# Performance work log

Measured on AMD Instinct MI355X. Metric: run time of the kernel, lower is better.

The kernel has to match this reference:

```python
import jax, jax.numpy as jnp
import numpy as np

N_NODES = 20000
N_EDGES = 320000


def cheb_conv(x, row, col, W, b):
    """PyG ChebConv with normalization='sym', lambda_max=2.0 (default).
    Scaled Laplacian L~ = L - I = -D^{-1/2} A D^{-1/2} (diagonal cancels:
    get_laplacian diag +1 plus add_self_loops fill -1).
    Tx_0 = x, Tx_1 = L~ x, Tx_k = 2 L~ Tx_{k-1} - Tx_{k-2};
    out = sum_k Tx_k @ W_k + b.
    """
    N = x.shape[0]
    mask = (row != col).astype(x.dtype)  # remove_self_loops
    deg = jax.ops.segment_sum(mask, row, num_segments=N)
    dis = jnp.where(deg > 0, 1.0 / jnp.sqrt(deg), 0.0)  # deg_inv_sqrt, inf->0
    w = -dis[row] * dis[col] * mask  # edge weights of L~ (diag entries are 0)

    def prop(t):  # y = L~ t via gather-scale-scatter over edges
        return jax.ops.segment_sum(w[:, None] * t[col], row, num_segments=N)

    K = W.shape[0]
    Tx0 = x
    out = Tx0 @ W[0]
    Tx1 = prop(Tx0)
    if K > 1:
        out = out + Tx1 @ W[1]
    for k in range(2, K):
        Tx2 = 2.0 * prop(Tx1) - Tx0
        out = out + Tx2 @ W[k]
        Tx0, Tx1 = Tx1, Tx2
    return out + b


def setup_inputs() -> dict:
    key = jax.random.key(0)
    ks = jax.random.split(key, 10)
    x = jax.random.normal(ks[0], (N_NODES, 1152), dtype=jnp.float32)
    row = jax.random.randint(ks[1], (N_EDGES,), 0, N_NODES)
    col = jax.random.randint(ks[2], (N_EDGES,), 0, N_NODES)
    s1 = 1.0 / np.sqrt(1152)
    s2 = 1.0 / np.sqrt(1152)
    s3 = 1.0 / np.sqrt(576)
    W1 = jax.random.normal(ks[3], (6, 1152, 1152), dtype=jnp.float32) * s1
    b1 = jax.random.normal(ks[4], (1152,), dtype=jnp.float32) * 0.01
    W2 = jax.random.normal(ks[5], (5, 1152, 576), dtype=jnp.float32) * s2
    b2 = jax.random.normal(ks[6], (576,), dtype=jnp.float32) * 0.01
    W3 = jax.random.normal(ks[7], (5, 576, 288), dtype=jnp.float32) * s3
    b3 = jax.random.normal(ks[8], (288,), dtype=jnp.float32) * 0.01
    return {"x": x, "row": row, "col": col, "W1": W1, "b1": b1,
            "W2": W2, "b2": b2, "W3": W3, "b3": b3}


def reference(x, row, col, W1, b1, W2, b2, W3, b3):
    # dropout(0.1) is identity in eval mode
    h = jax.nn.relu(cheb_conv(x, row, col, W1, b1))
    h = jax.nn.relu(cheb_conv(h, row, col, W2, b2))
    h = jax.nn.relu(cheb_conv(h, row, col, W3, b3))
    return h
```

## Files before the change

kernel.cpp:

```cpp
#include <hip/hip_runtime.h>
#include <hip/hip_bf16.h>

#define N_NODES 20000
#define N_EDGES 320000

typedef __attribute__((ext_vector_type(8))) short shortx8;
typedef __attribute__((ext_vector_type(4))) float floatx4;
using bf16 = __hip_bfloat16;

typedef __attribute__((address_space(1))) const unsigned int GuT;
typedef __attribute__((address_space(3))) unsigned int LuT;
__device__ __forceinline__ void gl2lds16(const bf16* g, bf16* l) {
  __builtin_amdgcn_global_load_lds((GuT*)g, (LuT*)l, 16, 0, 0);
}

__device__ inline float b2f(unsigned short u) {
  union { unsigned int i; float f; } x;
  x.i = ((unsigned int)u) << 16;
  return x.f;
}
__device__ inline unsigned short f2b(float f) {
  bf16 h(f);
  return *(unsigned short*)&h;
}

struct APtrs { const bf16* p[6]; };


__global__ void zero_kernel(int* p, int n) {
  int i = blockIdx.x * 256 + threadIdx.x;
  if (i < n) p[i] = 0;
}

__global__ void deg_kernel(const int* __restrict__ row, const int* __restrict__ col,
                           int* __restrict__ deg, int nE) {
  int e = blockIdx.x * 256 + threadIdx.x;
  if (e >= nE) return;
  int r = row[e], c = col[e];
  if (r != c) atomicAdd(&deg[r], 1);
}

__global__ void dis_kernel(const int* __restrict__ deg, float* __restrict__ dis, int n) {
  int i = blockIdx.x * 256 + threadIdx.x;
  if (i >= n) return;
  int d = deg[i];
  dis[i] = (d > 0) ? (1.0f / sqrtf((float)d)) : 0.0f;
}

__global__ __launch_bounds__(1024) void scan_kernel(const int* __restrict__ deg,
                                                    int* __restrict__ row_ptr,
                                                    int* __restrict__ cursor, int n) {
  __shared__ int part[1024];
  int t = threadIdx.x;
  int base = t * 20;
  int loc[20];
  int s = 0;
#pragma unroll
  for (int i = 0; i < 20; i++) {
    int idx = base + i;
    int v = (idx < n) ? deg[idx] : 0;
    loc[i] = s;
    s += v;
  }
  part[t] = s;
  __syncthreads();
  for (int offd = 1; offd < 1024; offd <<= 1) {
    int v = (t >= offd) ? part[t - offd] : 0;
    __syncthreads();
    part[t] += v;
    __syncthreads();
  }
  int basev = (t > 0) ? part[t - 1] : 0;
#pragma unroll
  for (int i = 0; i < 20; i++) {
    int idx = base + i;
    if (idx < n) {
      int rp = basev + loc[i];
      row_ptr[idx] = rp;
      cursor[idx] = rp;
    }
  }
  if (t == 1023) row_ptr[n] = part[1023];
}

__global__ void scatter_kernel(const int* __restrict__ row, const int* __restrict__ col,
                               const float* __restrict__ dis, int* __restrict__ cursor,
                               int* __restrict__ col_s, float* __restrict__ w_s, int nE) {
  int e = blockIdx.x * 256 + threadIdx.x;
  if (e >= nE) return;
  int r = row[e], c = col[e];
  if (r == c) return;
  int p = atomicAdd(&cursor[r], 1);
  col_s[p] = c;
  w_s[p] = -dis[r] * dis[c];
}


__global__ void wtrans_kernel(const float* __restrict__ W, bf16* __restrict__ Wt,
                              int K_, int I, int J) {
  __shared__ float tile[32][33];
  int jt = blockIdx.x % (J / 32);
  int rest = blockIdx.x / (J / 32);
  int it = rest % (I / 32);
  int k = rest / (I / 32);
  int tx = threadIdx.x, ty = threadIdx.y;
  const float* src = W + (size_t)k * I * J;
  for (int r = ty; r < 32; r += 8)
    tile[r][tx] = src[(size_t)(it * 32 + r) * J + jt * 32 + tx];
  __syncthreads();
  for (int r = ty; r < 32; r += 8) {
    int j = jt * 32 + r;
    Wt[((size_t)k * J + j) * I + it * 32 + tx] = bf16(tile[tx][r]);
  }
}


__global__ void cast_x_kernel(const float* __restrict__ x, bf16* __restrict__ dst, int n4) {
  int idx = blockIdx.x * 256 + threadIdx.x;
  if (idx >= n4) return;
  int flat = idx * 4;
  float4 v = *(const float4*)(x + flat);
  dst[flat + 0] = bf16(v.x);
  dst[flat + 1] = bf16(v.y);
  dst[flat + 2] = bf16(v.z);
  dst[flat + 3] = bf16(v.w);
}


template <int F, int VEC>
__global__ __launch_bounds__(320) void prop_kernel(
    const int* __restrict__ row_ptr, const int* __restrict__ col_s,
    const float* __restrict__ w_s, const bf16* __restrict__ src,
    const bf16* tx0, bf16* dst) {
  constexpr int C = F / VEC;
  int node = blockIdx.x;
  int t = threadIdx.x;
  bool act = t < C;
  int fb = t * VEC;
  int e0 = row_ptr[node], e1 = row_ptr[node + 1];
  float acc[VEC];
#pragma unroll
  for (int q = 0; q < VEC; q++) acc[q] = 0.0f;

  const unsigned short* sp = (const unsigned short*)src;
  int e = e0;
  for (; e + 16 <= e1; e += 16) {
    int cs[16];
    float wv[16];
#pragma unroll
    for (int u = 0; u < 16; u++) {
      cs[u] = col_s[e + u];
      wv[u] = w_s[e + u];
    }
    if (act) {
      if constexpr (VEC == 4) {
        ushort4 v[16];
#pragma unroll
        for (int u = 0; u < 16; u++) v[u] = *(const ushort4*)(sp + (size_t)cs[u] * F + fb);
#pragma unroll
        for (int u = 0; u < 16; u++) {
          acc[0] += wv[u] * b2f(v[u].x);
          acc[1] += wv[u] * b2f(v[u].y);
          acc[2] += wv[u] * b2f(v[u].z);
          acc[3] += wv[u] * b2f(v[u].w);
        }
      } else {
        ushort2 v[16];
#pragma unroll
        for (int u = 0; u < 16; u++) v[u] = *(const ushort2*)(sp + (size_t)cs[u] * F + fb);
#pragma unroll
        for (int u = 0; u < 16; u++) {
          acc[0] += wv[u] * b2f(v[u].x);
          acc[1] += wv[u] * b2f(v[u].y);
        }
      }
    }
  }
  for (; e + 4 <= e1; e += 4) {
    int cs[4];
    float wv[4];
#pragma unroll
    for (int u = 0; u < 4; u++) {
      cs[u] = col_s[e + u];
      wv[u] = w_s[e + u];
    }
    if (act) {
      if constexpr (VEC == 4) {
        ushort4 v[4];
#pragma unroll
        for (int u = 0; u < 4; u++) v[u] = *(const ushort4*)(sp + (size_t)cs[u] * F + fb);
#pragma unroll
        for (int u = 0; u < 4; u++) {
          acc[0] += wv[u] * b2f(v[u].x);
          acc[1] += wv[u] * b2f(v[u].y);
          acc[2] += wv[u] * b2f(v[u].z);
          acc[3] += wv[u] * b2f(v[u].w);
        }
      } else {
        ushort2 v[4];
#pragma unroll
        for (int u = 0; u < 4; u++) v[u] = *(const ushort2*)(sp + (size_t)cs[u] * F + fb);
#pragma unroll
        for (int u = 0; u < 4; u++) {
          acc[0] += wv[u] * b2f(v[u].x);
          acc[1] += wv[u] * b2f(v[u].y);
        }
      }
    }
  }
  for (; e < e1; e++) {
    int c = col_s[e];
    float w = w_s[e];
    if (act) {
      if constexpr (VEC == 4) {
        ushort4 v = *(const ushort4*)(sp + (size_t)c * F + fb);
        acc[0] += w * b2f(v.x);
        acc[1] += w * b2f(v.y);
        acc[2] += w * b2f(v.z);
        acc[3] += w * b2f(v.w);
      } else {
        ushort2 v = *(const ushort2*)(sp + (size_t)c * F + fb);
        acc[0] += w * b2f(v.x);
        acc[1] += w * b2f(v.y);
      }
    }
  }

  if (!act) return;
  unsigned short* dp = (unsigned short*)dst + (size_t)node * F + fb;
  if (tx0) {
    const unsigned short* t0 = (const unsigned short*)tx0 + (size_t)node * F + fb;
    if constexpr (VEC == 4) {
      ushort4 tv = *(const ushort4*)t0;
      ushort4 o;
      o.x = f2b(2.0f * acc[0] - b2f(tv.x));
      o.y = f2b(2.0f * acc[1] - b2f(tv.y));
      o.z = f2b(2.0f * acc[2] - b2f(tv.z));
      o.w = f2b(2.0f * acc[3] - b2f(tv.w));
      *(ushort4*)dp = o;
    } else {
      ushort2 tv = *(const ushort2*)t0;
      ushort2 o;
      o.x = f2b(2.0f * acc[0] - b2f(tv.x));
      o.y = f2b(2.0f * acc[1] - b2f(tv.y));
      *(ushort2*)dp = o;
    }
  } else {
    if constexpr (VEC == 4) {
      ushort4 o;
      o.x = f2b(acc[0]);
      o.y = f2b(acc[1]);
      o.z = f2b(acc[2]);
      o.w = f2b(acc[3]);
      *(ushort4*)dp = o;
    } else {
      ushort2 o;
      o.x = f2b(acc[0]);
      o.y = f2b(acc[1]);
      *(ushort2*)dp = o;
    }
  }
}


template <int MODE, int NSEG>
__global__ __launch_bounds__(256) void gemm_kernel(
    APtrs ap, const bf16* __restrict__ Bbase,
    const float* __restrict__ bias, float* __restrict__ accbuf,
    void* __restrict__ dst, int M, int Nout, int Kt, int dstLd) {
  __shared__ bf16 As[128 * 32];
  __shared__ bf16 Bs[128 * 32];
  int nb = (Nout + 127) >> 7;
  int mtiles = (M + 127) >> 7;
  int xcd = blockIdx.x & 7;
  int s = blockIdx.x >> 3;
  int bn = s % nb;
  int bm = (s / nb) * 8 + xcd;
  if (bm >= mtiles) return;
  int m0 = bm << 7, n0 = bn << 7;
  int t = threadIdx.x;
  int lane = t & 63;
  int wave = t >> 6;
  int wm = wave & 1, wn = wave >> 1;
  int l16 = lane & 15;
  int q4 = lane >> 4;
  floatx4 acc[4][4] = {};

  int srow = lane >> 2;
  int scol = (((lane & 3) ^ ((srow >> 1) & 3)) << 3);

#pragma unroll
  for (int seg = 0; seg < NSEG; seg++) {
    const bf16* A = ap.p[seg];
    const bf16* Bt = Bbase + (size_t)seg * Nout * Kt;
#pragma unroll 1
    for (int kt = 0; kt < Kt; kt += 32) {
#pragma unroll
      for (int q = 0; q < 2; q++) {
        int inst = (wave << 1) + q;
        int r = (inst << 4) + srow;
        int ga = m0 + r;
        if (ga < M)
          gl2lds16(A + (size_t)ga * Kt + kt + scol, &As[inst << 9]);
        int gb = n0 + r;
        if (gb < Nout)
          gl2lds16(Bt + (size_t)gb * Kt + kt + scol, &Bs[inst << 9]);
      }
      __syncthreads();
      shortx8 af[4], bfr[4];
#pragma unroll
      for (int i = 0; i < 4; i++) {
        int r = (wm << 6) + (i << 4) + l16;
        af[i] = *(const shortx8*)&As[(r << 5) + ((q4 ^ ((r >> 1) & 3)) << 3)];
      }
#pragma unroll
      for (int j = 0; j < 4; j++) {
        int r = (wn << 6) + (j << 4) + l16;
        bfr[j] = *(const shortx8*)&Bs[(r << 5) + ((q4 ^ ((r >> 1) & 3)) << 3)];
      }
#pragma unroll
      for (int i = 0; i < 4; i++)
#pragma unroll
        for (int j = 0; j < 4; j++)
          acc[i][j] = __builtin_amdgcn_mfma_f32_16x16x32_bf16(af[i], bfr[j], acc[i][j], 0, 0, 0);
      __syncthreads();
    }
  }

  int lq = lane >> 4;
#pragma unroll
  for (int j = 0; j < 4; j++) {
    int colg = n0 + (wn << 6) + (j << 4) + l16;
    if (colg >= Nout) continue;
    float bv = (MODE == 0 || MODE == 4 || MODE == 5) ? bias[colg] : 0.0f;
#pragma unroll
    for (int i = 0; i < 4; i++) {
      int rowb = m0 + (wm << 6) + (i << 4) + (lq << 2);
#pragma unroll
      for (int q = 0; q < 4; q++) {
        int rowg = rowb + q;
        if (rowg >= M) continue;
        float v = acc[i][j][q];
        size_t aidx = (size_t)rowg * Nout + colg;
        if constexpr (MODE == 0) {
          accbuf[aidx] = v + bv;
        } else if constexpr (MODE == 1) {
          accbuf[aidx] += v;
        } else if constexpr (MODE == 2) {
          float s2 = fmaxf(accbuf[aidx] + v, 0.0f);
          ((bf16*)dst)[(size_t)rowg * dstLd + colg] = bf16(s2);
        } else if constexpr (MODE == 3) {
          float s2 = fmaxf(accbuf[aidx] + v, 0.0f);
          ((float*)dst)[(size_t)rowg * Nout + colg] = s2;
        } else if constexpr (MODE == 4) {
          float s2 = fmaxf(v + bv, 0.0f);
          ((bf16*)dst)[(size_t)rowg * dstLd + colg] = bf16(s2);
        } else {
          float s2 = fmaxf(v + bv, 0.0f);
          ((float*)dst)[(size_t)rowg * Nout + colg] = s2;
        }
      }
    }
  }
}


extern "C" void kernel_launch(void* const* d_in, const int* in_sizes, int n_in,
                              void* d_out, int out_size, void* d_ws, size_t ws_size,
                              hipStream_t stream) {
  const float* x = (const float*)d_in[0];
  const int* row = (const int*)d_in[1];
  const int* col = (const int*)d_in[2];
  const float* W1 = (const float*)d_in[3];
  const float* b1 = (const float*)d_in[4];
  const float* W2 = (const float*)d_in[5];
  const float* b2 = (const float*)d_in[6];
  const float* W3 = (const float*)d_in[7];
  const float* b3 = (const float*)d_in[8];

  char* ws = (char*)d_ws;
  size_t off = 0;
  auto alloc = [&](size_t bytes) -> void* {
    void* p = ws + off;
    off += (bytes + 255) & ~(size_t)255;
    return p;
  };

  const size_t TXB = (size_t)N_NODES * 1152 * 2;
  bf16* Wt = (bf16*)alloc((size_t)6 * 1152 * 1152 * 2);
  int* deg = (int*)alloc(N_NODES * 4);
  float* dis = (float*)alloc(N_NODES * 4);
  int* row_ptr = (int*)alloc((N_NODES + 1) * 4);
  int* cursor = (int*)alloc(N_NODES * 4);
  int* col_s = (int*)alloc(N_EDGES * 4);
  float* w_s = (float*)alloc(N_EDGES * 4);
  size_t off_common = off;

  size_t need_A = off_common + 7 * ((TXB + 255) & ~(size_t)255);
  size_t need_B = off_common + 3 * ((TXB + 255) & ~(size_t)255) +
                  (((size_t)N_NODES * 1152 * 4 + 255) & ~(size_t)255);
  int tier = (ws_size >= need_A) ? 0 : (ws_size >= need_B) ? 1 : 2;

  zero_kernel<<<(N_NODES + 255) / 256, 256, 0, stream>>>(deg, N_NODES);
  deg_kernel<<<(N_EDGES + 255) / 256, 256, 0, stream>>>(row, col, deg, N_EDGES);
  dis_kernel<<<(N_NODES + 255) / 256, 256, 0, stream>>>(deg, dis, N_NODES);
  scan_kernel<<<1, 1024, 0, stream>>>(deg, row_ptr, cursor, N_NODES);
  scatter_kernel<<<(N_EDGES + 255) / 256, 256, 0, stream>>>(row, col, dis, cursor,
                                                            col_s, w_s, N_EDGES);

  const int MT = (N_NODES + 127) >> 7;
  const int GMT = 8 * ((MT + 7) >> 3);
  const bf16* NB = nullptr;
  const int NX = N_NODES * 1152 / 4;

  auto prop1152 = [&](const bf16* src, const bf16* tx0, bf16* dst) {
    prop_kernel<1152, 4><<<N_NODES, 320, 0, stream>>>(row_ptr, col_s, w_s, src, tx0, dst);
  };
  auto prop576 = [&](const bf16* src, const bf16* tx0, bf16* dst) {
    prop_kernel<576, 2><<<N_NODES, 320, 0, stream>>>(row_ptr, col_s, w_s, src, tx0, dst);
  };

  if (tier == 0) {
    bf16* T[7];
    for (int i = 0; i < 7; i++) T[i] = (bf16*)alloc(TXB);

    wtrans_kernel<<<6 * 36 * 36, dim3(32, 8), 0, stream>>>(W1, Wt, 6, 1152, 1152);
    cast_x_kernel<<<(NX + 255) / 256, 256, 0, stream>>>(x, T[0], NX);
    prop1152(T[0], NB, T[1]);
    prop1152(T[1], T[0], T[2]);
    prop1152(T[2], T[1], T[3]);
    prop1152(T[3], T[2], T[4]);
    prop1152(T[4], T[3], T[5]);
    {
      APtrs a = {{T[0], T[1], T[2], T[3], T[4], T[5]}};
      gemm_kernel<4, 6><<<GMT * 9, 256, 0, stream>>>(a, Wt, b1, nullptr, T[6],
                                                     N_NODES, 1152, 1152, 1152);
    }

    wtrans_kernel<<<5 * 36 * 18, dim3(32, 8), 0, stream>>>(W2, Wt, 5, 1152, 576);
    prop1152(T[6], NB, T[0]);
    prop1152(T[0], T[6], T[1]);
    prop1152(T[1], T[0], T[2]);
    prop1152(T[2], T[1], T[3]);
    {
      APtrs a = {{T[6], T[0], T[1], T[2], T[3], nullptr}};
      gemm_kernel<4, 5><<<GMT * 5, 256, 0, stream>>>(a, Wt, b2, nullptr, T[4],
                                                     N_NODES, 576, 1152, 576);
    }

    wtrans_kernel<<<5 * 18 * 9, dim3(32, 8), 0, stream>>>(W3, Wt, 5, 576, 288);
    prop576(T[4], NB, T[5]);
    prop576(T[5], T[4], T[0]);
    prop576(T[0], T[5], T[1]);
    prop576(T[1], T[0], T[2]);
    {
      APtrs a = {{T[4], T[5], T[0], T[1], T[2], nullptr}};
      gemm_kernel<5, 5><<<GMT * 3, 256, 0, stream>>>(a, Wt, b3, nullptr, d_out,
                                                     N_NODES, 288, 576, 0);
    }
    return;
  }

  bf16* TxP = (bf16*)alloc(TXB);
  bf16* TxQ = (bf16*)alloc(TXB);
  bf16* Th = (tier == 1) ? (bf16*)alloc(TXB) : nullptr;
  float* accb = (float*)alloc((size_t)N_NODES * 1152 * 4);
  if (off > ws_size) return;

  wtrans_kernel<<<6 * 36 * 36, dim3(32, 8), 0, stream>>>(W1, Wt, 6, 1152, 1152);
  cast_x_kernel<<<(NX + 255) / 256, 256, 0, stream>>>(x, TxP, NX);
  {
    const int F = 1152, NO = 1152, nb = 9;
    size_t wsl = (size_t)NO * F;
    prop1152(TxP, NB, TxQ);
    APtrs a01 = {{TxP, TxQ}};
    gemm_kernel<0, 2><<<GMT * nb, 256, 0, stream>>>(a01, Wt, b1, accb, nullptr,
                                                    N_NODES, NO, F, 0);
    prop1152(TxQ, TxP, TxP);
    prop1152(TxP, TxQ, TxQ);
    APtrs a23 = {{TxP, TxQ}};
    gemm_kernel<1, 2><<<GMT * nb, 256, 0, stream>>>(a23, Wt + 2 * wsl, b1, accb, nullptr,
                                                    N_NODES, NO, F, 0);
    prop1152(TxQ, TxP, TxP);
    prop1152(TxP, TxQ, TxQ);
    if (tier == 1) {
      APtrs a45 = {{TxP, TxQ}};
      gemm_kernel<2, 2><<<GMT * nb, 256, 0, stream>>>(a45, Wt + 4 * wsl, b1, accb, Th,
                                                      N_NODES, NO, F, 1152);
    } else {
      APtrs a4 = {{TxP}};
      gemm_kernel<1, 1><<<GMT * nb, 256, 0, stream>>>(a4, Wt + 4 * wsl, b1, accb, nullptr,
                                                      N_NODES, NO, F, 0);
      APtrs a5 = {{TxQ}};
      gemm_kernel<2, 1><<<GMT * nb, 256, 0, stream>>>(a5, Wt + 5 * wsl, b1, accb, TxP,
                                                      N_NODES, NO, F, 1152);
    }
  }

  bf16* h1 = (tier == 1) ? Th : TxP;
  bf16* u0 = (tier == 1) ? TxP : TxQ;
  bf16* u1 = (tier == 1) ? TxQ : TxP;

  wtrans_kernel<<<5 * 36 * 18, dim3(32, 8), 0, stream>>>(W2, Wt, 5, 1152, 576);
  {
    const int F = 1152, NO = 576, nb = 5;
    size_t wsl = (size_t)NO * F;
    prop1152(h1, NB, u0);
    APtrs a01 = {{h1, u0}};
    gemm_kernel<0, 2><<<GMT * nb, 256, 0, stream>>>(a01, Wt, b2, accb, nullptr,
                                                    N_NODES, NO, F, 0);
    prop1152(u0, h1, h1);
    prop1152(h1, u0, u0);
    APtrs a23 = {{h1, u0}};
    gemm_kernel<1, 2><<<GMT * nb, 256, 0, stream>>>(a23, Wt + 2 * wsl, b2, accb, nullptr,
                                                    N_NODES, NO, F, 0);
    prop1152(u0, h1, h1);
    APtrs a4 = {{h1}};
    gemm_kernel<2, 1><<<GMT * nb, 256, 0, stream>>>(a4, Wt + 4 * wsl, b2, accb, u0,
                                                    N_NODES, NO, F, 576);
  }

  bf16* h2 = u0;

  wtrans_kernel<<<5 * 18 * 9, dim3(32, 8), 0, stream>>>(W3, Wt, 5, 576, 288);
  {
    const int F = 576, NO = 288, nb = 3;
    size_t wsl = (size_t)NO * F;
    prop576(h2, NB, u1);
    APtrs a01 = {{h2, u1}};
    gemm_kernel<0, 2><<<GMT * nb, 256, 0, stream>>>(a01, Wt, b3, accb, nullptr,
                                                    N_NODES, NO, F, 0);
    prop576(u1, h2, h2);
    prop576(h2, u1, u1);
    APtrs a23 = {{h2, u1}};
    gemm_kernel<1, 2><<<GMT * nb, 256, 0, stream>>>(a23, Wt + 2 * wsl, b3, accb, nullptr,
                                                    N_NODES, NO, F, 0);
    prop576(u1, h2, h2);
    APtrs a4 = {{h2}};
    gemm_kernel<3, 1><<<GMT * nb, 256, 0, stream>>>(a4, Wt + 4 * wsl, b3, accb, d_out,
                                                    N_NODES, NO, F, 0);
  }
}
```

Before: 2.120 ms.

## Reorder layers 2 and 3 to GEMM first, then Clenshaw propagation on narrower outputs

For layers 2 and 3, the change first multiplies the input by all K weight slices in one wide GEMM, producing G_k = X W_k. It then evaluates the Chebyshev sum with a Clenshaw-style backward recurrence, running the sparse propagation on output-width features (576 or 288) instead of input width (1152 or 576). A new cprop kernel fuses the gather-scatter with the recurrence update and the final bias+ReLU. This halves the feature width of the memory-bound sparse passes. The trade-off is a wider GEMM output buffer and an extra bf16 rounding of the intermediates.

New measurement: 1.794 ms. 1.18x faster.

```diff
diff --git a/kernel.cpp b/kernel.cpp
--- a/kernel.cpp
+++ b/kernel.cpp
@@ -259,6 +259,101 @@
       o.y = f2b(acc[1]);
       *(ushort2*)dp = o;
     }
+  }
+}
+
+
+template <int F, int VEC, int BLK, int OUT>
+__global__ __launch_bounds__(BLK) void cprop_kernel(
+    const int* __restrict__ row_ptr, const int* __restrict__ col_s,
+    const float* __restrict__ w_s, const bf16* __restrict__ src,
+    const bf16* g, const bf16* sub, void* dstv, int ld, int dstLd,
+    float alpha, const float* __restrict__ bias) {
+  constexpr int C = F / VEC;
+  int node = blockIdx.x;
+  int t = threadIdx.x;
+  bool act = t < C;
+  int fb = t * VEC;
+  int e0 = row_ptr[node], e1 = row_ptr[node + 1];
+  float acc[VEC];
+#pragma unroll
+  for (int q = 0; q < VEC; q++) acc[q] = 0.0f;
+
+  const unsigned short* sp = (const unsigned short*)src;
+  int e = e0;
+  for (; e + 16 <= e1; e += 16) {
+    int cs[16];
+    float wv[16];
+#pragma unroll
+    for (int u = 0; u < 16; u++) {
+      cs[u] = col_s[e + u];
+      wv[u] = w_s[e + u];
+    }
+    if (act) {
+      ushort2 v[16];
+#pragma unroll
+      for (int u = 0; u < 16; u++) v[u] = *(const ushort2*)(sp + (size_t)cs[u] * ld + fb);
+#pragma unroll
+      for (int u = 0; u < 16; u++) {
+        acc[0] += wv[u] * b2f(v[u].x);
+        acc[1] += wv[u] * b2f(v[u].y);
+      }
+    }
+  }
+  for (; e + 4 <= e1; e += 4) {
+    int cs[4];
+    float wv[4];
+#pragma unroll
+    for (int u = 0; u < 4; u++) {
+      cs[u] = col_s[e + u];
+      wv[u] = w_s[e + u];
+    }
+    if (act) {
+      ushort2 v[4];
+#pragma unroll
+      for (int u = 0; u < 4; u++) v[u] = *(const ushort2*)(sp + (size_t)cs[u] * ld + fb);
+#pragma unroll
+      for (int u = 0; u < 4; u++) {
+        acc[0] += wv[u] * b2f(v[u].x);
+        acc[1] += wv[u] * b2f(v[u].y);
+      }
+    }
+  }
+  for (; e < e1; e++) {
+    int c = col_s[e];
+    float w = w_s[e];
+    if (act) {
+      ushort2 v = *(const ushort2*)(sp + (size_t)c * ld + fb);
+      acc[0] += w * b2f(v.x);
+      acc[1] += w * b2f(v.y);
+    }
+  }
+
+  if (!act) return;
+  const unsigned short* gp = (const unsigned short*)g + (size_t)node * ld + fb;
+  ushort2 gv = *(const ushort2*)gp;
+  float y0 = alpha * acc[0] + b2f(gv.x);
+  float y1 = alpha * acc[1] + b2f(gv.y);
+  if (sub) {
+    const unsigned short* su = (const unsigned short*)sub + (size_t)node * ld + fb;
+    ushort2 sv = *(const ushort2*)su;
+    y0 -= b2f(sv.x);
+    y1 -= b2f(sv.y);
+  }
+  if constexpr (OUT >= 1) {
+    y0 = fmaxf(y0 + bias[fb], 0.0f);
+    y1 = fmaxf(y1 + bias[fb + 1], 0.0f);
+  }
+  if constexpr (OUT == 2) {
+    float* dp = (float*)dstv + (size_t)node * dstLd + fb;
+    dp[0] = y0;
+    dp[1] = y1;
+  } else {
+    unsigned short* dp = (unsigned short*)dstv + (size_t)node * dstLd + fb;
+    ushort2 o;
+    o.x = f2b(y0);
+    o.y = f2b(y1);
+    *(ushort2*)dp = o;
   }
 }
 
@@ -355,9 +450,11 @@
         } else if constexpr (MODE == 4) {
           float s2 = fmaxf(v + bv, 0.0f);
           ((bf16*)dst)[(size_t)rowg * dstLd + colg] = bf16(s2);
-        } else {
+        } else if constexpr (MODE == 5) {
           float s2 = fmaxf(v + bv, 0.0f);
           ((float*)dst)[(size_t)rowg * Nout + colg] = s2;
+        } else {
+          ((bf16*)dst)[(size_t)rowg * dstLd + colg] = bf16(v);
         }
       }
     }
@@ -396,9 +493,8 @@
   float* w_s = (float*)alloc(N_EDGES * 4);
   size_t off_common = off;
 
-  size_t need_A = off_common + 7 * ((TXB + 255) & ~(size_t)255);
-  size_t need_B = off_common + 3 * ((TXB + 255) & ~(size_t)255) +
-                  (((size_t)N_NODES * 1152 * 4 + 255) & ~(size_t)255);
+  size_t need_A = off_common + 7 * TXB;
+  size_t need_B = off_common + 3 * TXB + (size_t)N_NODES * 1152 * 4 + 1024;
   int tier = (ws_size >= need_A) ? 0 : (ws_size >= need_B) ? 1 : 2;
 
   zero_kernel<<<(N_NODES + 255) / 256, 256, 0, stream>>>(deg, N_NODES);
@@ -438,25 +534,49 @@
     }
 
     wtrans_kernel<<<5 * 36 * 18, dim3(32, 8), 0, stream>>>(W2, Wt, 5, 1152, 576);
-    prop1152(T[6], NB, T[0]);
-    prop1152(T[0], T[6], T[1]);
-    prop1152(T[1], T[0], T[2]);
-    prop1152(T[2], T[1], T[3]);
+    bf16* g2 = T[0];
     {
-      APtrs a = {{T[6], T[0], T[1], T[2], T[3], nullptr}};
-      gemm_kernel<4, 5><<<GMT * 5, 256, 0, stream>>>(a, Wt, b2, nullptr, T[4],
-                                                     N_NODES, 576, 1152, 576);
+      APtrs a = {{T[6]}};
+      gemm_kernel<6, 1><<<GMT * 23, 256, 0, stream>>>(a, Wt, b2, nullptr, g2,
+                                                      N_NODES, 2880, 1152, 2880);
+    }
+    {
+      bf16* G0 = g2;
+      bf16* G1 = g2 + 576;
+      bf16* G2 = g2 + 2 * 576;
+      bf16* G3 = g2 + 3 * 576;
+      bf16* G4 = g2 + 4 * 576;
+      cprop_kernel<576, 2, 320, 0><<<N_NODES, 320, 0, stream>>>(
+          row_ptr, col_s, w_s, G4, G3, NB, G3, 2880, 2880, 2.0f, nullptr);
+      cprop_kernel<576, 2, 320, 0><<<N_NODES, 320, 0, stream>>>(
+          row_ptr, col_s, w_s, G3, G2, G4, G2, 2880, 2880, 2.0f, nullptr);
+      cprop_kernel<576, 2, 320, 0><<<N_NODES, 320, 0, stream>>>(
+          row_ptr, col_s, w_s, G2, G1, G3, G1, 2880, 2880, 2.0f, nullptr);
+      cprop_kernel<576, 2, 320, 1><<<N_NODES, 320, 0, stream>>>(
+          row_ptr, col_s, w_s, G1, G0, G2, T[3], 2880, 576, 1.0f, b2);
     }
 
     wtrans_kernel<<<5 * 18 * 9, dim3(32, 8), 0, stream>>>(W3, Wt, 5, 576, 288);
-    prop576(T[4], NB, T[5]);
-    prop576(T[5], T[4], T[0]);
-    prop576(T[0], T[5], T[1]);
-    prop576(T[1], T[0], T[2]);
+    bf16* g3 = T[4];
     {
-      APtrs a = {{T[4], T[5], T[0], T[1], T[2], nullptr}};
-      gemm_kernel<5, 5><<<GMT * 3, 256, 0, stream>>>(a, Wt, b3, nullptr, d_out,
-                                                     N_NODES, 288, 576, 0);
+      APtrs a = {{T[3]}};
+      gemm_kernel<6, 1><<<GMT * 12, 256, 0, stream>>>(a, Wt, b3, nullptr, g3,
+                                                      N_NODES, 1440, 576, 1440);
+    }
+    {
+      bf16* G0 = g3;
+      bf16* G1 = g3 + 288;
+      bf16* G2 = g3 + 2 * 288;
+      bf16* G3 = g3 + 3 * 288;
+      bf16* G4 = g3 + 4 * 288;
+      cprop_kernel<288, 2, 192, 0><<<N_NODES, 192, 0, stream>>>(
+          row_ptr, col_s, w_s, G4, G3, NB, G3, 1440, 1440, 2.0f, nullptr);
+      cprop_kernel<288, 2, 192, 0><<<N_NODES, 192, 0, stream>>>(
+          row_ptr, col_s, w_s, G3, G2, G4, G2, 1440, 1440, 2.0f, nullptr);
+      cprop_kernel<288, 2, 192, 0><<<N_NODES, 192, 0, stream>>>(
+          row_ptr, col_s, w_s, G2, G1, G3, G1, 1440, 1440, 2.0f, nullptr);
+      cprop_kernel<288, 2, 192, 2><<<N_NODES, 192, 0, stream>>>(
+          row_ptr, col_s, w_s, G1, G0, G2, d_out, 1440, 288, 1.0f, b3);
     }
     return;
   }
```
